# Performance work log

Hardware: AMD Instinct MI355X
Metric: run time of the kernel (lower is better)

The kernel has to match this reference:

```python
import jax, jax.numpy as jnp
import numpy as np

H = 64  # hidden_size
IN = 9  # input_size == output_size
PRED_LEN = 10
SRC_LEN = 7
B = 65536


def _lstm_step(x, h, c, Wih, Whh, b):
    # PyTorch gate order: i, f, g, o
    gates = x @ Wih.T + h @ Whh.T + b  # (B, 4H)
    i, f, g, o = jnp.split(gates, 4, axis=-1)
    i = jax.nn.sigmoid(i)
    f = jax.nn.sigmoid(f)
    g = jnp.tanh(g)
    o = jax.nn.sigmoid(o)
    c_new = f * c + i * g
    h_new = o * jnp.tanh(c_new)
    return h_new, c_new


def setup_inputs() -> dict:
    key = jax.random.key(0)
    ks = jax.random.split(key, 9)
    s = 1.0 / np.sqrt(H)  # torch LSTM init scale
    return {
        "src": jax.random.normal(ks[0], (B, SRC_LEN, IN), dtype=jnp.float32),
        "enc_Wih": jax.random.normal(ks[1], (4 * H, IN), dtype=jnp.float32) * s,
        "enc_Whh": jax.random.normal(ks[2], (4 * H, H), dtype=jnp.float32) * s,
        "enc_b": jax.random.normal(ks[3], (4 * H,), dtype=jnp.float32) * s,
        "dec_Wih": jax.random.normal(ks[4], (4 * H, IN), dtype=jnp.float32) * s,
        "dec_Whh": jax.random.normal(ks[5], (4 * H, H), dtype=jnp.float32) * s,
        "dec_b": jax.random.normal(ks[6], (4 * H,), dtype=jnp.float32) * s,
        "fc_W": jax.random.normal(ks[7], (IN, H), dtype=jnp.float32) * s,
        "fc_b": jax.random.normal(ks[8], (IN,), dtype=jnp.float32) * s,
    }


def reference(src, enc_Wih, enc_Whh, enc_b, dec_Wih, dec_Whh, dec_b, fc_W, fc_b):
    b = src.shape[0]
    h0 = jnp.zeros((b, H), dtype=src.dtype)
    c0 = jnp.zeros((b, H), dtype=src.dtype)

    # Encoder: scan over the 7 source timesteps
    def enc_f(carry, x_t):
        h, c = carry
        h, c = _lstm_step(x_t, h, c, enc_Wih, enc_Whh, enc_b)
        return (h, c), None

    (h, c), _ = jax.lax.scan(enc_f, (h0, c0), jnp.swapaxes(src, 0, 1))

    x_last = src[:, -1, :]  # (B, IN)

    def dec_f(carry, _):
        h, c, x = carry
        h, c = _lstm_step(x, h, c, dec_Wih, dec_Whh, dec_b)
        pred = h @ fc_W.T + fc_b  # (B, IN)
        return (h, c, pred), pred

    _, preds = jax.lax.scan(dec_f, (h, c, x_last), None, length=PRED_LEN)
    return jnp.swapaxes(preds, 0, 1)  # (B, PRED_LEN, IN)
```

## Files before the change

### kernel.cpp

```cpp
#include <hip/hip_runtime.h>
#include <hip/hip_bf16.h>
#include <stdint.h>

namespace {
constexpr int kH = 64;
constexpr int kIn = 9;
constexpr int kSrcLen = 7;
constexpr int kPredLen = 10;
constexpr int kRows = 64;
constexpr int kThreads = 256;
constexpr int kChunks = kRows / 16;
constexpr int kOutW = kPredLen * kIn;
constexpr int kABlk = 8;
constexpr int kASz = kABlk * kRows * 8;
constexpr int kAxSz = kRows * 16;

constexpr float kLog2e = 1.4426950408889634f;

typedef __attribute__((ext_vector_type(8))) _Float16 frag_a;
typedef __attribute__((ext_vector_type(4))) _Float16 frag_a2;
typedef __attribute__((ext_vector_type(4))) float frag_cd;

__device__ __forceinline__ float fast_rcp(float x) { return __builtin_amdgcn_rcpf(x); }
__device__ __forceinline__ float exp2_f(float x) { return __builtin_amdgcn_exp2f(x); }
__device__ __forceinline__ float sigmoid_pre(float x) { return fast_rcp(1.0f + exp2_f(-x)); }
__device__ __forceinline__ float tanh_pre(float x) { return 1.0f - 2.0f * fast_rcp(exp2_f(x) + 1.0f); }
__device__ __forceinline__ float tanh_f(float x) { return tanh_pre(x * (2.0f * kLog2e)); }

__device__ __forceinline__ float ldf(const void* p, int i, int isbf) {
  if (isbf) {
    uint32_t w = ((uint32_t)((const uint16_t*)p)[i]) << 16;
    float f; __builtin_memcpy(&f, &w, 4); return f;
  }
  return ((const float*)p)[i];
}
}

extern "C" __global__ void detect_dtype_kernel(const uint16_t* __restrict__ src_u16,
                                               int* __restrict__ flag) {
  const int t = threadIdx.x;
  int bad = 0;
  for (int i = t; i < 256; i += 64) {
    const uint16_t u = src_u16[i];
    const uint32_t e = (u >> 7) & 0xFF;
    const int plausible = (u == 0) || (e >= 100 && e <= 150);
    bad += !plausible;
  }
#pragma unroll
  for (int off = 32; off; off >>= 1) bad += __shfl_down(bad, off, 64);
  if (t == 0) *flag = (bad < 64) ? 1 : 0;
}

extern "C" __global__ void __launch_bounds__(kThreads)
__attribute__((amdgpu_waves_per_eu(4, 8)))
lstm_seq2seq_kernel(const void* __restrict__ src,
                    const void* __restrict__ enc_Wih,
                    const void* __restrict__ enc_Whh,
                    const void* __restrict__ enc_b,
                    const void* __restrict__ dec_Wih,
                    const void* __restrict__ dec_Whh,
                    const void* __restrict__ dec_b,
                    const void* __restrict__ fc_W,
                    const void* __restrict__ fc_b,
                    void* __restrict__ out,
                    const int* __restrict__ flag) {
  __shared__ __align__(16) _Float16 a_m[2][kASz];
  __shared__ __align__(16) _Float16 ax[kAxSz];

  const int tid = threadIdx.x;
  const int lane = tid & 63;
  const int wave = tid >> 6;
  const int quad = lane >> 4;
  const int half = lane & 15;
  const int row0 = blockIdx.x * kRows;
  const int isbf = *flag;
  const int col = wave * 16 + half;

  for (int i = tid; i < kASz; i += kThreads) {
    a_m[0][i] = (_Float16)0.0f;
    a_m[1][i] = (_Float16)0.0f;
  }
  for (int i = tid; i < kAxSz; i += kThreads) ax[i] = (_Float16)0.0f;

  float c_st[4 * kChunks];
#pragma unroll
  for (int i = 0; i < 4 * kChunks; ++i) c_st[i] = 0.0f;

  frag_a bm0[4], bm1[4];
  frag_a2 bm2[4];
  float bacc[4] = {0.f, 0.f, 0.f, 0.f};

  auto load_gate_frags = [&](const void* Whh, const void* Wih, const void* bv) {
#pragma unroll
    for (int nt = 0; nt < 4; ++nt) {
      const float scale = (nt == 2) ? (2.0f * kLog2e) : kLog2e;
      const int n = nt * kH + col;
      frag_a f0, f1;
#pragma unroll
      for (int j = 0; j < 8; ++j) {
        f0[j] = (_Float16)(scale * ldf(Whh, n * kH + (quad * 8 + j), isbf));
        f1[j] = (_Float16)(scale * ldf(Whh, n * kH + (32 + quad * 8 + j), isbf));
      }
      bm0[nt] = f0;
      bm1[nt] = f1;
      frag_a2 f2;
#pragma unroll
      for (int j = 0; j < 4; ++j) {
        const int k2 = quad * 4 + j;
        float v = 0.0f;
        if (k2 < kIn) v = ldf(Wih, n * kIn + k2, isbf);
        f2[j] = (_Float16)(scale * v);
      }
      bm2[nt] = f2;
      bacc[nt] = scale * ldf(bv, n, isbf);
    }
  };

  auto load_xfrags = [&](int s, frag_a2 (&xf)[kChunks]) {
#pragma unroll
    for (int ch = 0; ch < kChunks; ++ch) {
      frag_a2 f = {(_Float16)0.f, (_Float16)0.f, (_Float16)0.f, (_Float16)0.f};
      const int r = row0 + ch * 16 + half;
      const int base = r * (kSrcLen * kIn) + s * kIn;
      if (quad < 2) {
#pragma unroll
        for (int j = 0; j < 4; ++j) f[j] = (_Float16)ldf(src, base + quad * 4 + j, isbf);
      } else if (quad == 2) {
        f[0] = (_Float16)ldf(src, base + 8, isbf);
      }
      xf[ch] = f;
    }
  };

  auto lstm_step = [&](int cur, const frag_a2* xf) {
#pragma unroll 1
    for (int ch = 0; ch < kChunks; ++ch) {
      const int r = ch * 16 + half;
      const frag_a a0 = *(const frag_a*)&a_m[cur][((0 * 4 + quad) * kRows + r) * 8];
      const frag_a a1 = *(const frag_a*)&a_m[cur][((1 * 4 + quad) * kRows + r) * 8];
      const frag_a2 a2 = xf ? xf[ch] : *(const frag_a2*)&ax[r * 16 + quad * 4];

      frag_cd acc[4];
#pragma unroll
      for (int nt = 0; nt < 4; ++nt) {
        frag_cd a = {bacc[nt], bacc[nt], bacc[nt], bacc[nt]};
        a = __builtin_amdgcn_mfma_f32_16x16x32_f16(a0, bm0[nt], a, 0, 0, 0);
        a = __builtin_amdgcn_mfma_f32_16x16x32_f16(a1, bm1[nt], a, 0, 0, 0);
        a = __builtin_amdgcn_mfma_f32_16x16x16f16(a2, bm2[nt], a, 0, 0, 0);
        acc[nt] = a;
      }

#pragma unroll
      for (int j = 0; j < 4; ++j) {
        const float gi = acc[0][j];
        const float gf = acc[1][j];
        const float gg = acc[2][j];
        const float go = acc[3][j];
        float c = c_st[ch * 4 + j];
        c = fmaf(sigmoid_pre(gf), c, sigmoid_pre(gi) * tanh_pre(gg));
        c_st[ch * 4 + j] = c;
        const float h = sigmoid_pre(go) * tanh_f(c);
        const int rr = ch * 16 + quad * 4 + j;
        a_m[cur ^ 1][(((col >> 3) * kRows) + rr) * 8 + (col & 7)] = (_Float16)h;
      }
    }
  };

  load_gate_frags(enc_Whh, enc_Wih, enc_b);
  __syncthreads();

  int cur = 0;
  frag_a2 xf[kChunks];
#pragma unroll 1
  for (int s = 0; s < kSrcLen; ++s) {
    load_xfrags(s, xf);
    lstm_step(cur, xf);
    __syncthreads();
    cur ^= 1;
  }

  load_gate_frags(dec_Whh, dec_Wih, dec_b);
  load_xfrags(kSrcLen - 1, xf);
  lstm_step(cur, xf);
  __syncthreads();
  cur ^= 1;

  frag_a fm[2];
#pragma unroll
  for (int kt = 0; kt < 2; ++kt) {
    frag_a f;
#pragma unroll
    for (int j = 0; j < 8; ++j) {
      const int k = kt * 32 + quad * 8 + j;
      f[j] = (half < kIn) ? (_Float16)ldf(fc_W, half * kH + k, isbf) : (_Float16)0.0f;
    }
    fm[kt] = f;
  }
  const float fcb = (half < kIn) ? ldf(fc_b, half, isbf) : 0.0f;

  auto fc_head = [&](int t, int cb) {
    const int r = wave * 16 + half;
    const frag_a a0 = *(const frag_a*)&a_m[cb][((0 * 4 + quad) * kRows + r) * 8];
    const frag_a a1 = *(const frag_a*)&a_m[cb][((1 * 4 + quad) * kRows + r) * 8];
    frag_cd p = {fcb, fcb, fcb, fcb};
    p = __builtin_amdgcn_mfma_f32_16x16x32_f16(a0, fm[0], p, 0, 0, 0);
    p = __builtin_amdgcn_mfma_f32_16x16x32_f16(a1, fm[1], p, 0, 0, 0);
    if (half < kIn) {
#pragma unroll
      for (int j = 0; j < 4; ++j) {
        const int rr = wave * 16 + quad * 4 + j;
        const float pred = p[j];
        const int oidx = (row0 + rr) * kOutW + t * kIn + half;
        if (isbf) ((__hip_bfloat16*)out)[oidx] = __float2bfloat16(pred);
        else ((float*)out)[oidx] = pred;
        ax[rr * 16 + half] = (_Float16)pred;
      }
    }
  };

  fc_head(0, cur);
  __syncthreads();

#pragma unroll 1
  for (int t = 1; t < kPredLen; ++t) {
    lstm_step(cur, nullptr);
    __syncthreads();
    cur ^= 1;
    fc_head(t, cur);
    __syncthreads();
  }
}

extern "C" void kernel_launch(void* const* d_in, const int* in_sizes, int n_in,
                              void* d_out, int out_size, void* d_ws, size_t ws_size,
                              hipStream_t stream) {
  (void)n_in; (void)ws_size; (void)out_size;
  int* flag = (int*)d_ws;

  hipLaunchKernelGGL(detect_dtype_kernel, dim3(1), dim3(64), 0, stream,
                     (const uint16_t*)d_in[0], flag);

  const int b_total = in_sizes[0] / (kSrcLen * kIn);
  const int grid = b_total / kRows;

  hipLaunchKernelGGL(lstm_seq2seq_kernel, dim3(grid), dim3(kThreads), 0, stream,
                     d_in[0], d_in[1], d_in[2], d_in[3], d_in[4], d_in[5],
                     d_in[6], d_in[7], d_in[8], d_out, flag);
}
```

Baseline: 258.4 us.

## Give each wave its own rows and stage gate weights in LDS

Reorganizes work so each wave owns 16 batch rows and computes all 256 gate columns, instead of each wave owning a 16-column slice of all 64 rows. This removes the block-wide __syncthreads between timesteps, since the h state and predictions stay in per-wave LDS buffers. The weights now sit in shared memory and are reloaded as B fragments every step, not held in registers. The bias is folded into the x MFMA through a constant-1 input column, and the gate nonlinearities are merged to use fewer reciprocals. The trade-off is more LDS reads per step and a different occupancy hint.

```diff
diff --git a/kernel.cpp b/kernel.cpp
--- a/kernel.cpp
+++ b/kernel.cpp
@@ -7,15 +7,18 @@
 constexpr int kIn = 9;
 constexpr int kSrcLen = 7;
 constexpr int kPredLen = 10;
-constexpr int kRows = 64;
+constexpr int kRowsPerWave = 16;
+constexpr int kWaves = 4;
+constexpr int kRows = kRowsPerWave * kWaves;
 constexpr int kThreads = 256;
-constexpr int kChunks = kRows / 16;
 constexpr int kOutW = kPredLen * kIn;
-constexpr int kABlk = 8;
-constexpr int kASz = kABlk * kRows * 8;
-constexpr int kAxSz = kRows * 16;
+
+constexpr int kWStride = 80;
+constexpr int kTStride = 68;
+constexpr int kPStride = 20;
 
 constexpr float kLog2e = 1.4426950408889634f;
+constexpr float k2Log2e = 2.8853900817779268f;
 
 typedef __attribute__((ext_vector_type(8))) _Float16 frag_a;
 typedef __attribute__((ext_vector_type(4))) _Float16 frag_a2;
@@ -23,9 +26,6 @@
 
 __device__ __forceinline__ float fast_rcp(float x) { return __builtin_amdgcn_rcpf(x); }
 __device__ __forceinline__ float exp2_f(float x) { return __builtin_amdgcn_exp2f(x); }
-__device__ __forceinline__ float sigmoid_pre(float x) { return fast_rcp(1.0f + exp2_f(-x)); }
-__device__ __forceinline__ float tanh_pre(float x) { return 1.0f - 2.0f * fast_rcp(exp2_f(x) + 1.0f); }
-__device__ __forceinline__ float tanh_f(float x) { return tanh_pre(x * (2.0f * kLog2e)); }
 
 __device__ __forceinline__ float ldf(const void* p, int i, int isbf) {
   if (isbf) {
@@ -52,7 +52,7 @@
 }
 
 extern "C" __global__ void __launch_bounds__(kThreads)
-__attribute__((amdgpu_waves_per_eu(4, 8)))
+__attribute__((amdgpu_waves_per_eu(3, 4)))
 lstm_seq2seq_kernel(const void* __restrict__ src,
                     const void* __restrict__ enc_Wih,
                     const void* __restrict__ enc_Whh,
@@ -64,170 +64,155 @@
                     const void* __restrict__ fc_b,
                     void* __restrict__ out,
                     const int* __restrict__ flag) {
-  __shared__ __align__(16) _Float16 a_m[2][kASz];
-  __shared__ __align__(16) _Float16 ax[kAxSz];
+  __shared__ __align__(16) _Float16 Wl[4 * kH * kWStride];
+  __shared__ __align__(16) _Float16 Tb[kWaves][kRowsPerWave * kTStride];
+  __shared__ __align__(16) _Float16 Pb[kWaves][kRowsPerWave * kPStride];
 
   const int tid = threadIdx.x;
   const int lane = tid & 63;
   const int wave = tid >> 6;
   const int quad = lane >> 4;
   const int half = lane & 15;
-  const int row0 = blockIdx.x * kRows;
+  const int rw0 = blockIdx.x * kRows + wave * kRowsPerWave;
   const int isbf = *flag;
-  const int col = wave * 16 + half;
-
-  for (int i = tid; i < kASz; i += kThreads) {
-    a_m[0][i] = (_Float16)0.0f;
-    a_m[1][i] = (_Float16)0.0f;
-  }
-  for (int i = tid; i < kAxSz; i += kThreads) ax[i] = (_Float16)0.0f;
-
-  float c_st[4 * kChunks];
-#pragma unroll
-  for (int i = 0; i < 4 * kChunks; ++i) c_st[i] = 0.0f;
-
-  frag_a bm0[4], bm1[4];
-  frag_a2 bm2[4];
-  float bacc[4] = {0.f, 0.f, 0.f, 0.f};
-
-  auto load_gate_frags = [&](const void* Whh, const void* Wih, const void* bv) {
-#pragma unroll
-    for (int nt = 0; nt < 4; ++nt) {
-      const float scale = (nt == 2) ? (2.0f * kLog2e) : kLog2e;
-      const int n = nt * kH + col;
-      frag_a f0, f1;
-#pragma unroll
-      for (int j = 0; j < 8; ++j) {
-        f0[j] = (_Float16)(scale * ldf(Whh, n * kH + (quad * 8 + j), isbf));
-        f1[j] = (_Float16)(scale * ldf(Whh, n * kH + (32 + quad * 8 + j), isbf));
+
+  _Float16* Tw = &Tb[wave][0];
+  _Float16* Pw = &Pb[wave][0];
+
+  for (int i = lane; i < kRowsPerWave * kTStride; i += 64) Tw[i] = (_Float16)0.0f;
+  for (int i = lane; i < kRowsPerWave * kPStride; i += 64)
+    Pw[i] = ((i % kPStride) == kIn) ? (_Float16)1.0f : (_Float16)0.0f;
+
+  float c_st[16];
+#pragma unroll
+  for (int i = 0; i < 16; ++i) c_st[i] = 0.0f;
+
+  auto load_W = [&](const void* Whh, const void* Wih, const void* bv) {
+    const int n = tid;
+    const float scale = ((n >> 6) == 2) ? k2Log2e : kLog2e;
+    _Float16* wr = &Wl[n * kWStride];
+#pragma unroll 4
+    for (int k = 0; k < kH; ++k)
+      wr[k] = (_Float16)(scale * ldf(Whh, n * kH + k, isbf));
+#pragma unroll
+    for (int k = 0; k < 16; ++k) {
+      float v = 0.0f;
+      if (k < kIn) v = ldf(Wih, n * kIn + k, isbf);
+      else if (k == kIn) v = ldf(bv, n, isbf);
+      wr[kH + k] = (_Float16)(scale * v);
+    }
+  };
+
+  auto a2_src = [&](int s) -> frag_a2 {
+    frag_a2 f = {(_Float16)0.f, (_Float16)0.f, (_Float16)0.f, (_Float16)0.f};
+    const int base = (rw0 + half) * (kSrcLen * kIn) + s * kIn;
+    if (quad < 2) {
+#pragma unroll
+      for (int e = 0; e < 4; ++e) f[e] = (_Float16)ldf(src, base + quad * 4 + e, isbf);
+    } else if (quad == 2) {
+      f[0] = (_Float16)ldf(src, base + 8, isbf);
+      f[1] = (_Float16)1.0f;
+    }
+    return f;
+  };
+
+  auto lstm_step = [&](frag_a2 a2) {
+    const int tbase = half * kTStride + quad * 8;
+    const frag_a2 t0 = *(const frag_a2*)&Tw[tbase];
+    const frag_a2 t1 = *(const frag_a2*)&Tw[tbase + 4];
+    const frag_a2 t2 = *(const frag_a2*)&Tw[tbase + 32];
+    const frag_a2 t3 = *(const frag_a2*)&Tw[tbase + 36];
+    const frag_a a0 = __builtin_shufflevector(t0, t1, 0, 1, 2, 3, 4, 5, 6, 7);
+    const frag_a a1 = __builtin_shufflevector(t2, t3, 0, 1, 2, 3, 4, 5, 6, 7);
+#pragma unroll 1
+    for (int ct = 0; ct < 4; ++ct) {
+      frag_cd acc[4];
+#pragma unroll
+      for (int g = 0; g < 4; ++g) {
+        const int nb = (g * kH + ct * 16 + half) * kWStride;
+        const frag_a b0 = *(const frag_a*)&Wl[nb + quad * 8];
+        const frag_a b1 = *(const frag_a*)&Wl[nb + 32 + quad * 8];
+        const frag_a2 b2 = *(const frag_a2*)&Wl[nb + 64 + quad * 4];
+        frag_cd a = {0.f, 0.f, 0.f, 0.f};
+        a = __builtin_amdgcn_mfma_f32_16x16x32_f16(a0, b0, a, 0, 0, 0);
+        a = __builtin_amdgcn_mfma_f32_16x16x32_f16(a1, b1, a, 0, 0, 0);
+        a = __builtin_amdgcn_mfma_f32_16x16x16f16(a2, b2, a, 0, 0, 0);
+        acc[g] = a;
       }
-      bm0[nt] = f0;
-      bm1[nt] = f1;
-      frag_a2 f2;
-#pragma unroll
-      for (int j = 0; j < 4; ++j) {
-        const int k2 = quad * 4 + j;
-        float v = 0.0f;
-        if (k2 < kIn) v = ldf(Wih, n * kIn + k2, isbf);
-        f2[j] = (_Float16)(scale * v);
-      }
-      bm2[nt] = f2;
-      bacc[nt] = scale * ldf(bv, n, isbf);
-    }
-  };
-
-  auto load_xfrags = [&](int s, frag_a2 (&xf)[kChunks]) {
-#pragma unroll
-    for (int ch = 0; ch < kChunks; ++ch) {
-      frag_a2 f = {(_Float16)0.f, (_Float16)0.f, (_Float16)0.f, (_Float16)0.f};
-      const int r = row0 + ch * 16 + half;
-      const int base = r * (kSrcLen * kIn) + s * kIn;
-      if (quad < 2) {
-#pragma unroll
-        for (int j = 0; j < 4; ++j) f[j] = (_Float16)ldf(src, base + quad * 4 + j, isbf);
-      } else if (quad == 2) {
-        f[0] = (_Float16)ldf(src, base + 8, isbf);
-      }
-      xf[ch] = f;
-    }
-  };
-
-  auto lstm_step = [&](int cur, const frag_a2* xf) {
-#pragma unroll 1
-    for (int ch = 0; ch < kChunks; ++ch) {
-      const int r = ch * 16 + half;
-      const frag_a a0 = *(const frag_a*)&a_m[cur][((0 * 4 + quad) * kRows + r) * 8];
-      const frag_a a1 = *(const frag_a*)&a_m[cur][((1 * 4 + quad) * kRows + r) * 8];
-      const frag_a2 a2 = xf ? xf[ch] : *(const frag_a2*)&ax[r * 16 + quad * 4];
-
-      frag_cd acc[4];
-#pragma unroll
-      for (int nt = 0; nt < 4; ++nt) {
-        frag_cd a = {bacc[nt], bacc[nt], bacc[nt], bacc[nt]};
-        a = __builtin_amdgcn_mfma_f32_16x16x32_f16(a0, bm0[nt], a, 0, 0, 0);
-        a = __builtin_amdgcn_mfma_f32_16x16x32_f16(a1, bm1[nt], a, 0, 0, 0);
-        a = __builtin_amdgcn_mfma_f32_16x16x16f16(a2, bm2[nt], a, 0, 0, 0);
-        acc[nt] = a;
-      }
-
 #pragma unroll
       for (int j = 0; j < 4; ++j) {
         const float gi = acc[0][j];
         const float gf = acc[1][j];
         const float gg = acc[2][j];
         const float go = acc[3][j];
-        float c = c_st[ch * 4 + j];
-        c = fmaf(sigmoid_pre(gf), c, sigmoid_pre(gi) * tanh_pre(gg));
-        c_st[ch * 4 + j] = c;
-        const float h = sigmoid_pre(go) * tanh_f(c);
-        const int rr = ch * 16 + quad * 4 + j;
-        a_m[cur ^ 1][(((col >> 3) * kRows) + rr) * 8 + (col & 7)] = (_Float16)h;
+        const float ei = exp2_f(-gi);
+        const float ef = exp2_f(-gf);
+        const float eg = exp2_f(gg);
+        const float eo = exp2_f(-go);
+        const float c_old = c_st[ct * 4 + j];
+        const float p1 = (1.0f + ei) * (eg + 1.0f);
+        const float q = (eg - 1.0f) * (1.0f + ef);
+        const float num = fmaf(c_old, p1, q);
+        const float c = num * fast_rcp(p1 * (1.0f + ef));
+        c_st[ct * 4 + j] = c;
+        const float t = exp2_f(c * k2Log2e);
+        const float h = (t - 1.0f) * fast_rcp((1.0f + eo) * (t + 1.0f));
+        Tw[(quad * 4 + j) * kTStride + ct * 16 + half] = (_Float16)h;
       }
     }
   };
 
-  load_gate_frags(enc_Whh, enc_Wih, enc_b);
+  load_W(enc_Whh, enc_Wih, enc_b);
   __syncthreads();
 
-  int cur = 0;
-  frag_a2 xf[kChunks];
 #pragma unroll 1
-  for (int s = 0; s < kSrcLen; ++s) {
-    load_xfrags(s, xf);
-    lstm_step(cur, xf);
-    __syncthreads();
-    cur ^= 1;
-  }
-
-  load_gate_frags(dec_Whh, dec_Wih, dec_b);
-  load_xfrags(kSrcLen - 1, xf);
-  lstm_step(cur, xf);
+  for (int s = 0; s < kSrcLen; ++s) lstm_step(a2_src(s));
+
   __syncthreads();
-  cur ^= 1;
-
-  frag_a fm[2];
-#pragma unroll
-  for (int kt = 0; kt < 2; ++kt) {
-    frag_a f;
-#pragma unroll
-    for (int j = 0; j < 8; ++j) {
-      const int k = kt * 32 + quad * 8 + j;
-      f[j] = (half < kIn) ? (_Float16)ldf(fc_W, half * kH + k, isbf) : (_Float16)0.0f;
-    }
-    fm[kt] = f;
+  load_W(dec_Whh, dec_Wih, dec_b);
+  frag_a fm0, fm1;
+#pragma unroll
+  for (int j = 0; j < 8; ++j) {
+    fm0[j] = (half < kIn) ? (_Float16)ldf(fc_W, half * kH + j + quad * 8, isbf)
+                          : (_Float16)0.0f;
+    fm1[j] = (half < kIn) ? (_Float16)ldf(fc_W, half * kH + 32 + quad * 8 + j, isbf)
+                          : (_Float16)0.0f;
   }
   const float fcb = (half < kIn) ? ldf(fc_b, half, isbf) : 0.0f;
-
-  auto fc_head = [&](int t, int cb) {
-    const int r = wave * 16 + half;
-    const frag_a a0 = *(const frag_a*)&a_m[cb][((0 * 4 + quad) * kRows + r) * 8];
-    const frag_a a1 = *(const frag_a*)&a_m[cb][((1 * 4 + quad) * kRows + r) * 8];
+  __syncthreads();
+
+  auto fc_head = [&](int t) {
+    const int tbase = half * kTStride + quad * 8;
+    const frag_a2 t0 = *(const frag_a2*)&Tw[tbase];
+    const frag_a2 t1 = *(const frag_a2*)&Tw[tbase + 4];
+    const frag_a2 t2 = *(const frag_a2*)&Tw[tbase + 32];
+    const frag_a2 t3 = *(const frag_a2*)&Tw[tbase + 36];
+    const frag_a a0 = __builtin_shufflevector(t0, t1, 0, 1, 2, 3, 4, 5, 6, 7);
+    const frag_a a1 = __builtin_shufflevector(t2, t3, 0, 1, 2, 3, 4, 5, 6, 7);
     frag_cd p = {fcb, fcb, fcb, fcb};
-    p = __builtin_amdgcn_mfma_f32_16x16x32_f16(a0, fm[0], p, 0, 0, 0);
-    p = __builtin_amdgcn_mfma_f32_16x16x32_f16(a1, fm[1], p, 0, 0, 0);
+    p = __builtin_amdgcn_mfma_f32_16x16x32_f16(a0, fm0, p, 0, 0, 0);
+    p = __builtin_amdgcn_mfma_f32_16x16x32_f16(a1, fm1, p, 0, 0, 0);
     if (half < kIn) {
 #pragma unroll
       for (int j = 0; j < 4; ++j) {
-        const int rr = wave * 16 + quad * 4 + j;
+        const int rr = quad * 4 + j;
         const float pred = p[j];
-        const int oidx = (row0 + rr) * kOutW + t * kIn + half;
+        const int oidx = (rw0 + rr) * kOutW + t * kIn + half;
         if (isbf) ((__hip_bfloat16*)out)[oidx] = __float2bfloat16(pred);
         else ((float*)out)[oidx] = pred;
-        ax[rr * 16 + half] = (_Float16)pred;
+        Pw[rr * kPStride + half] = (_Float16)pred;
       }
     }
   };
 
-  fc_head(0, cur);
-  __syncthreads();
+  lstm_step(a2_src(kSrcLen - 1));
+  fc_head(0);
 
 #pragma unroll 1
   for (int t = 1; t < kPredLen; ++t) {
-    lstm_step(cur, nullptr);
-    __syncthreads();
-    cur ^= 1;
-    fc_head(t, cur);
-    __syncthreads();
+    const frag_a2 a2 = *(const frag_a2*)&Pw[half * kPStride + quad * 4];
+    lstm_step(a2);
+    fc_head(t);
   }
 }
 
```

Result: no change. 253.8 us (-1.8%).
